# Optimization experiments

Hardware: AMD Instinct MI355X
Metric: run time of the kernel (lower is better)

Reference implementation:

```python
import jax, jax.numpy as jnp
import numpy as np

RADIUS = 2
TOP_K = 8192
TEMPERATURE = 0.1
KSIZE = 2 * RADIUS + 1  # 5


def _hw_grid(dtype):
    # torch: meshgrid(x, x, 'ij') stacked, flattened row-major, cols swapped -> (dx, dy)
    x = jnp.linspace(-RADIUS, RADIUS, KSIZE, dtype=dtype)
    dy, dx = jnp.meshgrid(x, x, indexing='ij')  # dy varies over rows, dx over cols
    return jnp.stack([dx.reshape(-1), dy.reshape(-1)], axis=1)  # (k*k, 2) = (dx, dy)


def _nms2d(x):
    # kornia nms2d: local max pooling (stride 1, SAME padding with -inf), keep only peaks
    r = RADIUS
    xmax = jax.lax.reduce_window(
        x, -jnp.inf, jax.lax.max,
        window_dimensions=(1, 1, KSIZE, KSIZE),
        window_strides=(1, 1, 1, 1),
        padding=((0, 0), (0, 0), (r, r), (r, r)))
    return jnp.where(x == xmax, x, jnp.zeros_like(x))


def _bilinear_sample(img, xy):
    # F.grid_sample(mode='bilinear', align_corners=True) for in-range points.
    # img: (H, W); xy: (N, 2) normalized coords in [-1, 1], (x, y) order.
    H, W = img.shape
    px = (xy[:, 0] + 1.0) * 0.5 * (W - 1)
    py = (xy[:, 1] + 1.0) * 0.5 * (H - 1)
    x0 = jnp.clip(jnp.floor(px).astype(jnp.int32), 0, W - 1)
    y0 = jnp.clip(jnp.floor(py).astype(jnp.int32), 0, H - 1)
    x1 = jnp.clip(x0 + 1, 0, W - 1)
    y1 = jnp.clip(y0 + 1, 0, H - 1)
    wx = px - x0.astype(px.dtype)
    wy = py - y0.astype(py.dtype)
    v00 = img[y0, x0]; v01 = img[y0, x1]
    v10 = img[y1, x0]; v11 = img[y1, x1]
    return (v00 * (1 - wx) * (1 - wy) + v01 * wx * (1 - wy)
            + v10 * (1 - wx) * wy + v11 * wx * wy)


def setup_inputs() -> dict:
    key = jax.random.key(0)
    scores_map = jax.random.uniform(key, (8, 1, 2048, 2048), dtype=jnp.float32)
    return {"scores_map": scores_map}


def reference(scores_map):
    b, _, h, w = scores_map.shape
    r = RADIUS
    dtype = scores_map.dtype

    # --- NMS on detached scores, zero out borders (image_size=None branch) ---
    s_ng = jax.lax.stop_gradient(scores_map)
    nms = _nms2d(s_ng)
    nms = nms.at[:, :, :r, :].set(0.0).at[:, :, :, :r].set(0.0)
    nms = nms.at[:, :, h - r:, :].set(0.0).at[:, :, :, w - r:].set(0.0)

    # --- fixed top-k keypoint selection (top_k > 0 branch) ---
    _, idx = jax.lax.top_k(nms.reshape(b, -1), TOP_K)  # (b, K) flat indices
    ky_i = idx // w
    kx_i = idx % w

    # --- patch extraction == nn.Unfold(kernel, padding=radius) gathered at kpts ---
    padded = jnp.pad(scores_map[:, 0], ((0, 0), (r, r), (r, r)))  # zero pad
    di, dj = jnp.meshgrid(jnp.arange(KSIZE), jnp.arange(KSIZE), indexing='ij')
    di = di.reshape(-1); dj = dj.reshape(-1)  # row-major patch order (matches unfold)
    rows = ky_i[..., None] + di  # (b, K, k*k) ; +r offset absorbed by padding origin
    cols = kx_i[..., None] + dj
    patch = jax.vmap(lambda im, rr, cc: im[rr, cc])(padded, rows, cols)  # (b,K,k2)

    # --- soft-argmax sub-pixel refinement ---
    grid = _hw_grid(dtype)  # (k2, 2) as (dx, dy)
    max_v = jax.lax.stop_gradient(jnp.max(patch, axis=-1, keepdims=True))
    x_exp = jnp.exp((patch - max_v) / TEMPERATURE)       # (b, K, k2)
    x_sum = jnp.sum(x_exp, axis=-1, keepdims=True)       # (b, K, 1)
    xy_res = jnp.einsum('bkp,pc->bkc', x_exp, grid) / x_sum  # (b, K, 2)

    # score dispersity: weighted mean squared distance to the soft centroid
    delta = (grid[None, None, :, :] - xy_res[:, :, None, :]) / r  # (b,K,k2,2)
    dist2 = jnp.sum(delta * delta, axis=-1)                        # (b,K,k2)
    disp = jnp.sum(x_exp * dist2, axis=-1) / jnp.sum(x_exp, axis=-1)  # (b,K)

    # --- normalized keypoint coords and bilinear score resampling ---
    wh = jnp.array([w - 1, h - 1], dtype=dtype)
    kxy = jnp.stack([kx_i.astype(dtype), ky_i.astype(dtype)], axis=-1) + xy_res
    kxy = kxy / wh * 2.0 - 1.0  # (b, K, 2) in [-1, 1]
    kscore = jax.vmap(_bilinear_sample)(scores_map[:, 0], kxy)  # (b, K)

    return kxy, kscore, disp
```

## Files before the change

kernel.cpp:

```cpp
#include <hip/hip_runtime.h>

#define BATCH 8
#define HH 2048
#define WW 2048
#define NPIX (HH*WW)
#define TOPK 8192
#define NB 16384
#define PEAK_CAP 196608
#define CHUNK 32768
#define NCHUNK 6
#define FCHUNK 2048
#define LBINS 2048
#define LO_BIN (NB - LBINS)
#define CAND_CAP 16384

#define OFF_PEAKS  0ull
#define OFF_CANDS  (OFF_PEAKS + (size_t)BATCH*PEAK_CAP*8ull)
#define OFF_HIST   (OFF_CANDS + (size_t)BATCH*CAND_CAP*8ull)
#define OFF_SA     (OFF_HIST  + (size_t)BATCH*NB*4ull)
#define OFF_FILL   (OFF_SA    + (size_t)BATCH*NB*4ull)
#define OFF_PCOUNT (OFF_FILL  + (size_t)BATCH*NB*4ull)
#define OFF_NCAND  (OFF_PCOUNT + 64ull)
#define OFF_BSTAR  (OFF_NCAND + 64ull)
#define OFF_END    (OFF_PCOUNT + 192ull)
#define OFF_PART   (OFF_PCOUNT + 256ull)

__device__ __forceinline__ int bucket_of(float v) {
    int bk = (int)(v * 16384.0f);
    if (bk > NB - 1) bk = NB - 1;
    if (bk < 0) bk = 0;
    return bk;
}

__global__ __launch_bounds__(1024) void k_nms(
    const float* __restrict__ scores,
    unsigned long long* __restrict__ peaks,
    unsigned int* __restrict__ pcount)
{
    const int b = blockIdx.z;
    const int tx = threadIdx.x & 31;
    const int ty = threadIdx.x >> 5;
    const int x = blockIdx.x * 128 + tx * 4;
    const int y = blockIdx.y * 128 + ty * 4;
    const float* img = scores + (size_t)b * NPIX;
    const float4* imgq = (const float4*)img;

    __shared__ unsigned long long lbuf[2048];
    __shared__ unsigned int lcnt;
    __shared__ unsigned int lbase;
    if (threadIdx.x == 0) lcnt = 0;
    __syncthreads();

    const int q = x >> 2;
    const int qm = (q > 0) ? q - 1 : 0;
    const int qp = (q < WW / 4 - 1) ? q + 1 : WW / 4 - 1;

    float hm[8][4];
    float c4[4][4];

#pragma unroll
    for (int j = 0; j < 8; ++j) {
        int gy = y - 2 + j;
        gy = gy < 0 ? 0 : (gy > HH - 1 ? HH - 1 : gy);
        const float4* rowq = imgq + (size_t)gy * (WW / 4);
        const float4 A = rowq[qm];
        const float4 B = rowq[q];
        const float4 C = rowq[qp];
        const float v[12] = {A.x, A.y, A.z, A.w, B.x, B.y, B.z, B.w,
                             C.x, C.y, C.z, C.w};
        float aa[8];
#pragma unroll
        for (int k = 0; k < 8; ++k) aa[k] = fmaxf(v[k + 2], v[k + 3]);
#pragma unroll
        for (int i = 0; i < 4; ++i)
            hm[j][i] = fmaxf(fmaxf(aa[i], aa[i + 2]), v[i + 6]);
        if (j >= 2 && j <= 5) {
#pragma unroll
            for (int i = 0; i < 4; ++i) c4[j - 2][i] = v[i + 4];
        }
    }

#pragma unroll
    for (int r = 0; r < 4; ++r) {
        const int oy = y + r;
        const bool yok = (oy >= 2) && (oy <= HH - 3);
#pragma unroll
        for (int i = 0; i < 4; ++i) {
            const float vm = fmaxf(fmaxf(fmaxf(hm[r][i], hm[r + 1][i]),
                                         fmaxf(hm[r + 2][i], hm[r + 3][i])),
                                   hm[r + 4][i]);
            const float cv = c4[r][i];
            const int col = x + i;
            if (yok && col >= 2 && col <= WW - 3 && cv == vm) {
                unsigned int pos = atomicAdd(&lcnt, 1u);
                if (pos < 2048u) {
                    unsigned int idx = (unsigned int)(oy * WW + col);
                    lbuf[pos] = ((unsigned long long)__float_as_uint(cv) << 32) |
                                (unsigned long long)(~idx);
                }
            }
        }
    }
    __syncthreads();

    unsigned int cnt = lcnt;
    if (cnt > 2048u) cnt = 2048u;
    if (threadIdx.x == 0) lbase = atomicAdd(&pcount[b], cnt);
    __syncthreads();
    const unsigned int gbase = lbase;
    for (unsigned int s = threadIdx.x; s < cnt; s += 1024) {
        unsigned int gpos = gbase + s;
        if (gpos < PEAK_CAP) peaks[(size_t)b * PEAK_CAP + gpos] = lbuf[s];
    }
}

__global__ __launch_bounds__(1024) void k_hist(
    const unsigned long long* __restrict__ peaks,
    const unsigned int* __restrict__ pcount,
    unsigned int* __restrict__ partials)
{
    const int b = blockIdx.y;
    const int blk = blockIdx.x;
    unsigned int n = pcount[b];
    if (n > PEAK_CAP) n = PEAK_CAP;
    const unsigned int base = blk * CHUNK;
    if (base >= n) return;

    __shared__ unsigned int h[NB / 2];
    for (int w = threadIdx.x; w < NB / 2; w += 1024) h[w] = 0u;
    __syncthreads();

    const unsigned int end = (base + CHUNK < n) ? base + CHUNK : n;
    for (unsigned int i = base + threadIdx.x; i < end; i += 1024) {
        unsigned long long key = peaks[(size_t)b * PEAK_CAP + i];
        float v = __uint_as_float((unsigned int)(key >> 32));
        int bk = bucket_of(v);
        atomicAdd(&h[bk >> 1], (bk & 1) ? 0x10000u : 1u);
    }
    __syncthreads();

    unsigned int* dst = partials + ((size_t)(b * NCHUNK + blk)) * (NB / 2);
    for (int w = threadIdx.x; w < NB / 2; w += 1024) dst[w] = h[w];
}

__global__ __launch_bounds__(256) void k_scan(
    const unsigned int* __restrict__ partials,
    const unsigned int* __restrict__ pcount,
    unsigned int* __restrict__ hist,
    unsigned int* __restrict__ SA,
    unsigned int* __restrict__ fill,
    unsigned int* __restrict__ ncand,
    unsigned int* __restrict__ bstar)
{
    const int b = blockIdx.x;
    unsigned int n = pcount[b];
    if (n > PEAK_CAP) n = PEAK_CAP;
    const int nblk = (int)((n + CHUNK - 1) / CHUNK);
    unsigned int* sab = SA + b * NB;
    const int t = threadIdx.x;

    __shared__ unsigned int h[NB / 2];
    __shared__ unsigned int ps[256];
    __shared__ int bmax;

    for (int w = t; w < NB; w += 256) fill[b * NB + w] = 0u;

    for (int w = t; w < NB / 2; w += 256) {
        unsigned int lo = 0, hi = 0;
        for (int k = 0; k < nblk; ++k) {
            const unsigned int p = partials[((size_t)(b * NCHUNK + k)) * (NB / 2) + w];
            lo += p & 0xFFFFu;
            hi += p >> 16;
        }
        h[w] = lo | (hi << 16);
        ((uint2*)(hist + (size_t)b * NB))[w] = make_uint2(lo, hi);
    }
    __syncthreads();

    unsigned int sum = 0;
    for (int kk = 0; kk < 32; ++kk) {
        const int k = (kk + t) & 31;
        const unsigned int p = h[t * 32 + k];
        sum += (p & 0xFFFFu) + (p >> 16);
    }
    ps[t] = sum;
    __syncthreads();
    for (int off = 1; off < 256; off <<= 1) {
        unsigned int v = (t + off < 256) ? ps[t + off] : 0u;
        __syncthreads();
        ps[t] += v;
        __syncthreads();
    }
    const unsigned int run0 = ps[t] - sum;

    unsigned int run = run0;
    int bst_local = -1;
    for (int i = 63; i >= 0; --i) {
        const unsigned int w = h[t * 32 + (i >> 1)];
        const unsigned int hv = (i & 1) ? (w >> 16) : (w & 0xFFFFu);
        if (run + hv >= TOPK && bst_local < 0) bst_local = t * 64 + i;
        run += hv;
    }
    if (t == 0) bmax = -1;
    __syncthreads();
    if (bst_local >= 0) atomicMax(&bmax, bst_local);
    __syncthreads();
    const int Bs = bmax < 0 ? 0 : bmax;

    if (t * 64 + 63 >= Bs) {
        run = run0;
        for (int i = 63; i >= 0; --i) {
            const int bin = t * 64 + i;
            const unsigned int w = h[t * 32 + (i >> 1)];
            const unsigned int hv = (i & 1) ? (w >> 16) : (w & 0xFFFFu);
            if (bin >= Bs) sab[bin] = run;
            run += hv;
        }
    }
    __syncthreads();

    if (t == 0) {
        bstar[b] = (unsigned int)Bs;
        const unsigned int w = h[Bs >> 1];
        const unsigned int hv = (Bs & 1) ? (w >> 16) : (w & 0xFFFFu);
        unsigned int nc = sab[Bs] + hv;
        if (nc > CAND_CAP) nc = CAND_CAP;
        ncand[b] = nc;
    }
}

__global__ __launch_bounds__(256) void k_filter(
    const unsigned long long* __restrict__ peaks,
    const unsigned int* __restrict__ pcount,
    const unsigned int* __restrict__ bstar,
    const unsigned int* __restrict__ SA,
    unsigned int* __restrict__ fill,
    unsigned long long* __restrict__ cands)
{
    const int b = blockIdx.y;
    unsigned int n = pcount[b];
    if (n > PEAK_CAP) n = PEAK_CAP;
    const unsigned int base = blockIdx.x * FCHUNK;
    if (base >= n) return;
    const unsigned int end = (base + FCHUNK < n) ? base + FCHUNK : n;
    const unsigned int bs = bstar[b];
    const unsigned long long* pb = peaks + (size_t)b * PEAK_CAP;
    unsigned long long* cb = cands + (size_t)b * CAND_CAP;

    __shared__ unsigned long long wbuf[FCHUNK];
    __shared__ unsigned int cnt[LBINS];
    __shared__ unsigned int off[LBINS];
    __shared__ unsigned int nw;
    for (int j = threadIdx.x; j < LBINS; j += 256) { cnt[j] = 0u; off[j] = 0u; }
    if (threadIdx.x == 0) nw = 0u;
    __syncthreads();

    for (unsigned int i = base + threadIdx.x; i < end; i += 256) {
        const unsigned long long key = pb[i];
        const float v = __uint_as_float((unsigned int)(key >> 32));
        const int bk = bucket_of(v);
        if ((unsigned int)bk < bs) continue;
        if (bk >= LO_BIN) {
            const unsigned int p = atomicAdd(&nw, 1u);
            wbuf[p] = key;
            atomicAdd(&cnt[bk - LO_BIN], 1u);
        } else {
            unsigned int pos = SA[b * NB + bk] + atomicAdd(&fill[b * NB + bk], 1u);
            if (pos < CAND_CAP) cb[pos] = key;
        }
    }
    __syncthreads();

    for (int j = threadIdx.x; j < LBINS; j += 256) {
        const unsigned int c = cnt[j];
        if (c) cnt[j] = atomicAdd(&fill[b * NB + LO_BIN + j], c);
    }
    __syncthreads();

    const unsigned int w = nw;
    for (unsigned int i = threadIdx.x; i < w; i += 256) {
        const unsigned long long key = wbuf[i];
        const float v = __uint_as_float((unsigned int)(key >> 32));
        const int bk = bucket_of(v);
        const unsigned int l = atomicAdd(&off[bk - LO_BIN], 1u);
        const unsigned int pos = SA[b * NB + bk] + cnt[bk - LO_BIN] + l;
        if (pos < CAND_CAP) cb[pos] = key;
    }
}

__global__ __launch_bounds__(256) void k_out(
    const float* __restrict__ scores,
    const unsigned long long* __restrict__ cands,
    const unsigned int* __restrict__ ncand,
    const unsigned int* __restrict__ SA,
    const unsigned int* __restrict__ hist,
    float* __restrict__ out)
{
    const int b = blockIdx.y;
    unsigned int n = ncand[b];
    if (n > CAND_CAP) n = CAND_CAP;
    const int base = blockIdx.x * 256;
    const unsigned long long* cb = cands + (size_t)b * CAND_CAP;

    __shared__ unsigned long long seg[1024];
    for (int t = threadIdx.x; t < 1024; t += 256) {
        int gi = base - 384 + t;
        unsigned long long v = 0ull;
        if (gi >= 0 && gi < (int)n) v = cb[gi];
        seg[t] = v;
    }
    __syncthreads();

    unsigned int ci = base + threadIdx.x;
    if (ci >= n) return;

    const unsigned long long key = cb[ci];
    float v = __uint_as_float((unsigned int)(key >> 32));
    const int bk = bucket_of(v);
    const unsigned int seg0 = SA[b * NB + bk];
    const unsigned int len = hist[b * NB + bk];

    unsigned int r = 0;
    if ((int)seg0 >= base - 384 && (int)(seg0 + len) <= base + 640) {
        const int s0 = (int)seg0 - (base - 384);
        for (unsigned int j = 0; j < len; ++j)
            r += (seg[s0 + j] > key) ? 1u : 0u;
    } else {
#pragma unroll 4
        for (unsigned int j = 0; j < len; ++j)
            r += (cb[seg0 + j] > key) ? 1u : 0u;
    }
    const unsigned int rank = seg0 + r;
    if (rank >= TOPK) return;

    const unsigned int idx = ~((unsigned int)(key & 0xFFFFFFFFull));
    const int ky = (int)(idx >> 11);
    const int kx = (int)(idx & (WW - 1));
    const float* img = scores + (size_t)b * NPIX;

    float patch[25];
#pragma unroll
    for (int dy = 0; dy < 5; ++dy) {
#pragma unroll
        for (int dx = 0; dx < 5; ++dx) {
            patch[dy * 5 + dx] = img[(size_t)(ky + dy - 2) * WW + (kx + dx - 2)];
        }
    }
    float mx = patch[0];
#pragma unroll
    for (int p = 1; p < 25; ++p) mx = fmaxf(mx, patch[p]);

    float e[25];
    float s = 0.0f, sx = 0.0f, sy = 0.0f;
#pragma unroll
    for (int p = 0; p < 25; ++p) {
        float ex = expf((patch[p] - mx) * 10.0f);
        e[p] = ex;
        s += ex;
        sx += ex * (float)(p % 5 - 2);
        sy += ex * (float)(p / 5 - 2);
    }
    const float xx = sx / s;
    const float yy = sy / s;

    float dsum = 0.0f;
#pragma unroll
    for (int p = 0; p < 25; ++p) {
        float ddx = ((float)(p % 5 - 2) - xx) * 0.5f;
        float ddy = ((float)(p / 5 - 2) - yy) * 0.5f;
        dsum += e[p] * (ddx * ddx + ddy * ddy);
    }
    const float disp = dsum / s;

    const float kxy_x = ((float)kx + xx) / (float)(WW - 1) * 2.0f - 1.0f;
    const float kxy_y = ((float)ky + yy) / (float)(HH - 1) * 2.0f - 1.0f;

    const float px = (kxy_x + 1.0f) * 0.5f * (float)(WW - 1);
    const float py = (kxy_y + 1.0f) * 0.5f * (float)(HH - 1);
    int x0 = (int)floorf(px); x0 = x0 < 0 ? 0 : (x0 > WW - 1 ? WW - 1 : x0);
    int y0 = (int)floorf(py); y0 = y0 < 0 ? 0 : (y0 > HH - 1 ? HH - 1 : y0);
    int x1 = x0 + 1 > WW - 1 ? WW - 1 : x0 + 1;
    int y1 = y0 + 1 > HH - 1 ? HH - 1 : y0 + 1;
    const float wx = px - (float)x0;
    const float wy = py - (float)y0;
    const float v00 = img[(size_t)y0 * WW + x0];
    const float v01 = img[(size_t)y0 * WW + x1];
    const float v10 = img[(size_t)y1 * WW + x0];
    const float v11 = img[(size_t)y1 * WW + x1];
    const float ksc = v00 * (1.0f - wx) * (1.0f - wy) + v01 * wx * (1.0f - wy)
                    + v10 * (1.0f - wx) * wy + v11 * wx * wy;

    const size_t ok = (size_t)b * TOPK + rank;
    out[2 * ok]     = kxy_x;
    out[2 * ok + 1] = kxy_y;
    out[(size_t)BATCH * TOPK * 2 + ok] = ksc;
    out[(size_t)BATCH * TOPK * 3 + ok] = disp;
}

extern "C" void kernel_launch(void* const* d_in, const int* in_sizes, int n_in,
                              void* d_out, int out_size, void* d_ws, size_t ws_size,
                              hipStream_t stream) {
    const float* scores = (const float*)d_in[0];
    float* out = (float*)d_out;
    char* ws = (char*)d_ws;

    unsigned long long* peaks = (unsigned long long*)(ws + OFF_PEAKS);
    unsigned long long* cands = (unsigned long long*)(ws + OFF_CANDS);
    unsigned int* hist   = (unsigned int*)(ws + OFF_HIST);
    unsigned int* SA     = (unsigned int*)(ws + OFF_SA);
    unsigned int* fill   = (unsigned int*)(ws + OFF_FILL);
    unsigned int* pcount = (unsigned int*)(ws + OFF_PCOUNT);
    unsigned int* ncand  = (unsigned int*)(ws + OFF_NCAND);
    unsigned int* bstar  = (unsigned int*)(ws + OFF_BSTAR);
    unsigned int* part   = (unsigned int*)(ws + OFF_PART);

    hipMemsetAsync(ws + OFF_PCOUNT, 0, (size_t)(OFF_END - OFF_PCOUNT), stream);

    k_nms<<<dim3(WW / 128, HH / 128, BATCH), 1024, 0, stream>>>(scores, peaks, pcount);
    k_hist<<<dim3(NCHUNK, BATCH), 1024, 0, stream>>>(peaks, pcount, part);
    k_scan<<<dim3(BATCH), 256, 0, stream>>>(part, pcount, hist, SA, fill, ncand, bstar);
    k_filter<<<dim3(PEAK_CAP / FCHUNK, BATCH), 256, 0, stream>>>(peaks, pcount, bstar, SA, fill, cands);
    k_out<<<dim3(CAND_CAP / 256, BATCH), 256, 0, stream>>>(scores, cands, ncand, SA, hist, out);
}
```

Measured before the change: 318.5 us.

## Fuse histogram and scan kernels via last-block-done atomic counter

Merges the per-chunk histogram kernel and the per-batch scan kernel into one launch. Each block builds its partial histogram, then an atomic done counter picks the last block per batch, which reduces the partials and runs the prefix scan and threshold search with 1024 threads instead of 256. The fill-buffer zeroing is also spread across all chunk blocks. This removes one kernel launch and its gap, at the cost of threadfence-based inter-block synchronization and a serialized tail in one block.

```diff
diff --git a/kernel.cpp b/kernel.cpp
--- a/kernel.cpp
+++ b/kernel.cpp
@@ -22,7 +22,8 @@
 #define OFF_PCOUNT (OFF_FILL  + (size_t)BATCH*NB*4ull)
 #define OFF_NCAND  (OFF_PCOUNT + 64ull)
 #define OFF_BSTAR  (OFF_NCAND + 64ull)
-#define OFF_END    (OFF_PCOUNT + 192ull)
+#define OFF_DONE   (OFF_PCOUNT + 192ull)
+#define OFF_END    (OFF_PCOUNT + 256ull)
 #define OFF_PART   (OFF_PCOUNT + 256ull)
 
 __device__ __forceinline__ int bucket_of(float v) {
@@ -114,58 +115,60 @@
     }
 }
 
-__global__ __launch_bounds__(1024) void k_hist(
+__global__ __launch_bounds__(1024) void k_histscan(
     const unsigned long long* __restrict__ peaks,
     const unsigned int* __restrict__ pcount,
-    unsigned int* __restrict__ partials)
+    unsigned int* __restrict__ partials,
+    unsigned int* __restrict__ hist,
+    unsigned int* __restrict__ SA,
+    unsigned int* __restrict__ fill,
+    unsigned int* __restrict__ done,
+    unsigned int* __restrict__ ncand,
+    unsigned int* __restrict__ bstar)
 {
     const int b = blockIdx.y;
     const int blk = blockIdx.x;
+    const int tid = threadIdx.x;
     unsigned int n = pcount[b];
     if (n > PEAK_CAP) n = PEAK_CAP;
-    const unsigned int base = blk * CHUNK;
-    if (base >= n) return;
 
     __shared__ unsigned int h[NB / 2];
-    for (int w = threadIdx.x; w < NB / 2; w += 1024) h[w] = 0u;
-    __syncthreads();
-
-    const unsigned int end = (base + CHUNK < n) ? base + CHUNK : n;
-    for (unsigned int i = base + threadIdx.x; i < end; i += 1024) {
-        unsigned long long key = peaks[(size_t)b * PEAK_CAP + i];
-        float v = __uint_as_float((unsigned int)(key >> 32));
-        int bk = bucket_of(v);
-        atomicAdd(&h[bk >> 1], (bk & 1) ? 0x10000u : 1u);
-    }
-    __syncthreads();
-
-    unsigned int* dst = partials + ((size_t)(b * NCHUNK + blk)) * (NB / 2);
-    for (int w = threadIdx.x; w < NB / 2; w += 1024) dst[w] = h[w];
-}
-
-__global__ __launch_bounds__(256) void k_scan(
-    const unsigned int* __restrict__ partials,
-    const unsigned int* __restrict__ pcount,
-    unsigned int* __restrict__ hist,
-    unsigned int* __restrict__ SA,
-    unsigned int* __restrict__ fill,
-    unsigned int* __restrict__ ncand,
-    unsigned int* __restrict__ bstar)
-{
-    const int b = blockIdx.x;
-    unsigned int n = pcount[b];
-    if (n > PEAK_CAP) n = PEAK_CAP;
+    __shared__ unsigned int ps[1024];
+    __shared__ int bmax;
+    __shared__ unsigned int isLast;
+
+    {
+        const int per = (NB + NCHUNK - 1) / NCHUNK;
+        const int w0 = blk * per;
+        const int w1 = (w0 + per < NB) ? w0 + per : NB;
+        for (int w = w0 + tid; w < w1; w += 1024) fill[b * NB + w] = 0u;
+    }
+
+    const unsigned int base = (unsigned int)blk * CHUNK;
+    if (base < n) {
+        for (int w = tid; w < NB / 2; w += 1024) h[w] = 0u;
+        __syncthreads();
+        const unsigned int end = (base + CHUNK < n) ? base + CHUNK : n;
+        for (unsigned int i = base + tid; i < end; i += 1024) {
+            unsigned long long key = peaks[(size_t)b * PEAK_CAP + i];
+            float v = __uint_as_float((unsigned int)(key >> 32));
+            int bk = bucket_of(v);
+            atomicAdd(&h[bk >> 1], (bk & 1) ? 0x10000u : 1u);
+        }
+        __syncthreads();
+        unsigned int* dst = partials + ((size_t)(b * NCHUNK + blk)) * (NB / 2);
+        for (int w = tid; w < NB / 2; w += 1024) dst[w] = h[w];
+    }
+
+    __threadfence();
+    __syncthreads();
+    if (tid == 0) isLast = (atomicAdd(&done[b], 1u) == NCHUNK - 1) ? 1u : 0u;
+    __syncthreads();
+    if (!isLast) return;
+    __threadfence();
+
     const int nblk = (int)((n + CHUNK - 1) / CHUNK);
-    unsigned int* sab = SA + b * NB;
-    const int t = threadIdx.x;
-
-    __shared__ unsigned int h[NB / 2];
-    __shared__ unsigned int ps[256];
-    __shared__ int bmax;
-
-    for (int w = t; w < NB; w += 256) fill[b * NB + w] = 0u;
-
-    for (int w = t; w < NB / 2; w += 256) {
+    for (int w = tid; w < NB / 2; w += 1024) {
         unsigned int lo = 0, hi = 0;
         for (int k = 0; k < nblk; ++k) {
             const unsigned int p = partials[((size_t)(b * NCHUNK + k)) * (NB / 2) + w];
@@ -178,40 +181,41 @@
     __syncthreads();
 
     unsigned int sum = 0;
-    for (int kk = 0; kk < 32; ++kk) {
-        const int k = (kk + t) & 31;
-        const unsigned int p = h[t * 32 + k];
+    for (int kk = 0; kk < 8; ++kk) {
+        const int k = (kk + tid) & 7;
+        const unsigned int p = h[tid * 8 + k];
         sum += (p & 0xFFFFu) + (p >> 16);
     }
-    ps[t] = sum;
-    __syncthreads();
-    for (int off = 1; off < 256; off <<= 1) {
-        unsigned int v = (t + off < 256) ? ps[t + off] : 0u;
+    ps[tid] = sum;
+    __syncthreads();
+    for (int off = 1; off < 1024; off <<= 1) {
+        unsigned int v = (tid + off < 1024) ? ps[tid + off] : 0u;
         __syncthreads();
-        ps[t] += v;
+        ps[tid] += v;
         __syncthreads();
     }
-    const unsigned int run0 = ps[t] - sum;
+    const unsigned int run0 = ps[tid] - sum;
 
     unsigned int run = run0;
     int bst_local = -1;
-    for (int i = 63; i >= 0; --i) {
-        const unsigned int w = h[t * 32 + (i >> 1)];
+    for (int i = 15; i >= 0; --i) {
+        const unsigned int w = h[tid * 8 + (i >> 1)];
         const unsigned int hv = (i & 1) ? (w >> 16) : (w & 0xFFFFu);
-        if (run + hv >= TOPK && bst_local < 0) bst_local = t * 64 + i;
+        if (run + hv >= TOPK && bst_local < 0) bst_local = tid * 16 + i;
         run += hv;
     }
-    if (t == 0) bmax = -1;
+    if (tid == 0) bmax = -1;
     __syncthreads();
     if (bst_local >= 0) atomicMax(&bmax, bst_local);
     __syncthreads();
     const int Bs = bmax < 0 ? 0 : bmax;
 
-    if (t * 64 + 63 >= Bs) {
+    unsigned int* sab = SA + b * NB;
+    if (tid * 16 + 15 >= Bs) {
         run = run0;
-        for (int i = 63; i >= 0; --i) {
-            const int bin = t * 64 + i;
-            const unsigned int w = h[t * 32 + (i >> 1)];
+        for (int i = 15; i >= 0; --i) {
+            const int bin = tid * 16 + i;
+            const unsigned int w = h[tid * 8 + (i >> 1)];
             const unsigned int hv = (i & 1) ? (w >> 16) : (w & 0xFFFFu);
             if (bin >= Bs) sab[bin] = run;
             run += hv;
@@ -219,7 +223,7 @@
     }
     __syncthreads();
 
-    if (t == 0) {
+    if (tid == 0) {
         bstar[b] = (unsigned int)Bs;
         const unsigned int w = h[Bs >> 1];
         const unsigned int hv = (Bs & 1) ? (w >> 16) : (w & 0xFFFFu);
@@ -412,13 +416,13 @@
     unsigned int* pcount = (unsigned int*)(ws + OFF_PCOUNT);
     unsigned int* ncand  = (unsigned int*)(ws + OFF_NCAND);
     unsigned int* bstar  = (unsigned int*)(ws + OFF_BSTAR);
+    unsigned int* done   = (unsigned int*)(ws + OFF_DONE);
     unsigned int* part   = (unsigned int*)(ws + OFF_PART);
 
     hipMemsetAsync(ws + OFF_PCOUNT, 0, (size_t)(OFF_END - OFF_PCOUNT), stream);
 
     k_nms<<<dim3(WW / 128, HH / 128, BATCH), 1024, 0, stream>>>(scores, peaks, pcount);
-    k_hist<<<dim3(NCHUNK, BATCH), 1024, 0, stream>>>(peaks, pcount, part);
-    k_scan<<<dim3(BATCH), 256, 0, stream>>>(part, pcount, hist, SA, fill, ncand, bstar);
+    k_histscan<<<dim3(NCHUNK, BATCH), 1024, 0, stream>>>(peaks, pcount, part, hist, SA, fill, done, ncand, bstar);
     k_filter<<<dim3(PEAK_CAP / FCHUNK, BATCH), 256, 0, stream>>>(peaks, pcount, bstar, SA, fill, cands);
     k_out<<<dim3(CAND_CAP / 256, BATCH), 256, 0, stream>>>(scores, cands, ncand, SA, hist, out);
 }
```

Result: faster. 296.5 us (-6.9%).
